# Kernel tuning notes

Hardware: AMD Instinct MI355X
Metric: run time of the kernel (lower is better)

The kernel has to match this reference:

```python
import jax, jax.numpy as jnp
import numpy as np

B, T, C = 4, 2048, 1024
N_HEAD = 16
HEAD_DIM = C // N_HEAD
SCALE = 1.0 / np.sqrt(HEAD_DIM).astype(np.float32)


def setup_inputs() -> dict:
    key = jax.random.key(0)
    ks = jax.random.split(key, 5)
    std = 1.0 / np.sqrt(C).astype(np.float32)
    return {
        "x": jax.random.normal(ks[0], (B, T, C), dtype=jnp.float32),
        "Wq": jax.random.normal(ks[1], (C, C), dtype=jnp.float32) * std,
        "Wk": jax.random.normal(ks[2], (C, C), dtype=jnp.float32) * std,
        "Wv": jax.random.normal(ks[3], (C, C), dtype=jnp.float32) * std,
        "Wo": jax.random.normal(ks[4], (C, C), dtype=jnp.float32) * std,
    }


def reference(x, Wq, Wk, Wv, Wo):
    # nn.Linear(x) == x @ W.T; projections then split heads: (B, H, T, D)
    def split_heads(t):
        return t.reshape(B, T, N_HEAD, HEAD_DIM).transpose(0, 2, 1, 3)

    q = split_heads(x @ Wq.T)
    k = split_heads(x @ Wk.T)
    v = split_heads(x @ Wv.T)

    att = jnp.einsum("bhqd,bhkd->bhqk", q, k) * SCALE  # (B, H, T, T)
    causal = jnp.tril(jnp.ones((T, T), dtype=bool))
    att = jnp.where(causal[None, None], att, -jnp.inf)
    att = jax.nn.softmax(att, axis=-1)
    # dropout = 0.0 (eval): identity
    y = jnp.einsum("bhqk,bhkd->bhqd", att, v)  # (B, H, T, D)
    y = y.transpose(0, 2, 1, 3).reshape(B, T, C)
    return y @ Wo.T
```

## Files before the change

kernel.cpp:

```cpp
#include <hip/hip_runtime.h>
#include <stdint.h>

#define B_SZ   4
#define T_SEQ  2048
#define C_DIM  1024
#define N_HEAD 16
#define HEAD_D 64
#define QSCALE 0.18033688011112042f
#define M_FIX  12.0f

typedef unsigned short u16;
typedef unsigned int   u32;
typedef __bf16  bfv8  __attribute__((ext_vector_type(8)));
typedef float   f32x4 __attribute__((ext_vector_type(4)));

__device__ __forceinline__ u16 f2bf_hu(float f) {
  union { float f; u32 i; } u; u.f = f;
  return (u16)((u.i + 0x8000u) >> 16);
}
__device__ __forceinline__ u32 pkbf16(float a, float b) {
  union { float f; u32 i; } ua, ub; ua.f = a; ub.f = b;
  return ((ua.i + 0x8000u) >> 16) | ((ub.i + 0x8000u) & 0xFFFF0000u);
}
__device__ __forceinline__ float fexp2(float x) {
#if __has_builtin(__builtin_amdgcn_exp2f)
  return __builtin_amdgcn_exp2f(x);
#else
  return __expf(x * 0.69314718f);
#endif
}

__device__ __forceinline__ void async_cp16(const u16* __restrict__ g, u16* l) {
  __builtin_amdgcn_global_load_lds(
      (const __attribute__((address_space(1))) void*)g,
      (__attribute__((address_space(3))) void*)l, 16, 0, 0);
}

__global__ __launch_bounds__(256) void cvt_kernel(const float* __restrict__ src,
                                                  u16* __restrict__ dst, int n4) {
  int i = blockIdx.x * 256 + threadIdx.x;
  if (i < n4) {
    float4 v = ((const float4*)src)[i];
    int2 o; o.x = (int)pkbf16(v.x, v.y); o.y = (int)pkbf16(v.z, v.w);
    ((int2*)dst)[i] = o;
  }
}
__global__ __launch_bounds__(256) void cvt_w_kernel(
    const float* __restrict__ W0, const float* __restrict__ W1,
    const float* __restrict__ W2, const float* __restrict__ W3,
    u16* __restrict__ dst) {
  const float* s = (blockIdx.y == 0) ? W0 : (blockIdx.y == 1) ? W1
                 : (blockIdx.y == 2) ? W2 : W3;
  u16* d = dst + (size_t)blockIdx.y * (C_DIM * C_DIM);
  int i = blockIdx.x * 256 + threadIdx.x;
  float4 v = ((const float4*)s)[i];
  int2 o; o.x = (int)pkbf16(v.x, v.y); o.y = (int)pkbf16(v.z, v.w);
  ((int2*)d)[i] = o;
}

__device__ __forceinline__ void mfma_step(const u16* Sbuf, int wm, int wn,
                                          int frow, int fk, f32x4 acc[4][4]) {
  const u16* As = Sbuf;
  const u16* Bs = Sbuf + 4096;
  bfv8 af[4], bfr[4];
#pragma unroll
  for (int mt = 0; mt < 4; mt++)
    af[mt] = *(const bfv8*)(As + (wm * 64 + mt * 16 + frow) * 32 + fk);
#pragma unroll
  for (int nt = 0; nt < 4; nt++)
    bfr[nt] = *(const bfv8*)(Bs + (wn * 64 + nt * 16 + frow) * 32 + fk);
#pragma unroll
  for (int mt = 0; mt < 4; mt++)
#pragma unroll
    for (int nt = 0; nt < 4; nt++)
      acc[mt][nt] = __builtin_amdgcn_mfma_f32_16x16x32_bf16(
          af[mt], bfr[nt], acc[mt][nt], 0, 0, 0);
}

__device__ __forceinline__ void gemm_core(const u16* __restrict__ A,
                                          const u16* __restrict__ Bw,
                                          int m0, int n0,
                                          f32x4 acc[4][4],
                                          u16* smem) {
  const int tid  = threadIdx.x;
  const int wave = tid >> 6;
  const int lane = tid & 63;
  const int frow = lane & 15;
  const int fk   = (lane >> 4) * 8;
  const int wm   = wave >> 1, wn = wave & 1;

  const int lrow = tid >> 2;
  const int lcol = (tid & 3) * 8;
  const u16* ga0 = A  + (size_t)(m0 + lrow)      * C_DIM + lcol;
  const u16* ga1 = A  + (size_t)(m0 + 64 + lrow) * C_DIM + lcol;
  const u16* gb0 = Bw + (size_t)(n0 + lrow)      * C_DIM + lcol;
  const u16* gb1 = Bw + (size_t)(n0 + 64 + lrow) * C_DIM + lcol;
  u16* b0 = smem;
  u16* b1 = smem + 8192;
  const int so = tid * 8;

#define STAGE_TO(dst) do {                        \
    async_cp16(ga0, (dst) + so);                  \
    async_cp16(ga1, (dst) + 2048 + so);           \
    async_cp16(gb0, (dst) + 4096 + so);           \
    async_cp16(gb1, (dst) + 6144 + so);           \
    ga0 += 32; ga1 += 32; gb0 += 32; gb1 += 32;   \
  } while (0)

  STAGE_TO(b0);
  __syncthreads();

  for (int it = 0; it < 32; it += 2) {
    STAGE_TO(b1);
    mfma_step(b0, wm, wn, frow, fk, acc);
    __syncthreads();
    if (it < 30) STAGE_TO(b0);
    mfma_step(b1, wm, wn, frow, fk, acc);
    __syncthreads();
  }
#undef STAGE_TO
}

__global__ __launch_bounds__(256) void gemm_qkv_kernel(
    const u16* __restrict__ X, const u16* __restrict__ Wq,
    const u16* __restrict__ Wk, const u16* __restrict__ Wv,
    u16* __restrict__ Qo, u16* __restrict__ Ko, u16* __restrict__ Vo) {
  __shared__ __align__(16) u16 smem[16384];
  const u16* W = (blockIdx.z == 0) ? Wq : (blockIdx.z == 1) ? Wk : Wv;
  u16* dst     = (blockIdx.z == 0) ? Qo : (blockIdx.z == 1) ? Ko : Vo;
  const int m0 = blockIdx.x * 128, n0 = blockIdx.y * 128;

  f32x4 acc[4][4];
#pragma unroll
  for (int i = 0; i < 4; i++)
#pragma unroll
    for (int j = 0; j < 4; j++) acc[i][j] = {0.f, 0.f, 0.f, 0.f};

  gemm_core(X, W, m0, n0, acc, smem);
  __syncthreads();

  const int lane = threadIdx.x & 63, wave = threadIdx.x >> 6;
  const int wm = wave >> 1, wn = wave & 1;
  const int quad = lane >> 4, col = lane & 15;
  u16* buf = smem + wave * 4096;
  const int bb = (m0 + wm * 64) >> 11;
  const int t0 = (m0 + wm * 64) & (T_SEQ - 1);
  const int h  = (n0 >> 6) + wn;

  if (blockIdx.z == 2) {
#pragma unroll
    for (int mt = 0; mt < 4; mt++)
#pragma unroll
      for (int nt = 0; nt < 4; nt++) {
        int d_l = nt * 16 + col;
        int g   = mt * 4 + quad;
        int gp  = g ^ (d_l & 15);
        int2 o;
        o.x = (int)pkbf16(acc[mt][nt][0], acc[mt][nt][1]);
        o.y = (int)pkbf16(acc[mt][nt][2], acc[mt][nt][3]);
        *(int2*)(buf + d_l * 64 + gp * 4) = o;
      }
#pragma unroll
    for (int tt = 0; tt < 8; tt++) {
      int d_l = tt * 8 + (lane >> 3);
      int seg = lane & 7;
      int g0 = (2 * seg) ^ (d_l & 15), g1 = (2 * seg + 1) ^ (d_l & 15);
      int2 a  = *(const int2*)(buf + d_l * 64 + g0 * 4);
      int2 bv = *(const int2*)(buf + d_l * 64 + g1 * 4);
      int4 o; o.x = a.x; o.y = a.y; o.z = bv.x; o.w = bv.y;
      *(int4*)(Vo + (((size_t)(bb * N_HEAD + h) * HEAD_D + d_l) * T_SEQ
                     + t0 + seg * 8)) = o;
    }
  } else {
    const float sc = (blockIdx.z == 0) ? QSCALE : 1.0f;
#pragma unroll
    for (int mt = 0; mt < 4; mt++)
#pragma unroll
      for (int nt = 0; nt < 4; nt++)
#pragma unroll
        for (int r = 0; r < 4; r++) {
          int m_l = mt * 16 + quad * 4 + r;
          int n_l = nt * 16 + col;
          int gp = (n_l >> 3) ^ (m_l & 7);
          buf[m_l * 64 + gp * 8 + (n_l & 7)] = f2bf_hu(acc[mt][nt][r] * sc);
        }
#pragma unroll
    for (int tt = 0; tt < 8; tt++) {
      int m_l = tt * 8 + (lane >> 3);
      int seg = lane & 7;
      int gp = seg ^ (m_l & 7);
      int4 o = *(const int4*)(buf + m_l * 64 + gp * 8);
      *(int4*)(dst + (((size_t)(bb * N_HEAD + h) * T_SEQ + t0 + m_l) * HEAD_D
                      + seg * 8)) = o;
    }
  }
}

__global__ __launch_bounds__(256) void gemm_out_kernel(
    const u16* __restrict__ Y, const u16* __restrict__ Wo,
    float* __restrict__ Out) {
  __shared__ __align__(16) u16 smem[16384];
  const int m0 = blockIdx.x * 128, n0 = blockIdx.y * 128;

  f32x4 acc[4][4];
#pragma unroll
  for (int i = 0; i < 4; i++)
#pragma unroll
    for (int j = 0; j < 4; j++) acc[i][j] = {0.f, 0.f, 0.f, 0.f};

  gemm_core(Y, Wo, m0, n0, acc, smem);
  __syncthreads();

  const int lane = threadIdx.x & 63, wave = threadIdx.x >> 6;
  const int wm = wave >> 1, wn = wave & 1;
  const int quad = lane >> 4, col = lane & 15;
  float* bufF = (float*)(smem + wave * 4096);

#pragma unroll
  for (int c = 0; c < 2; c++) {
#pragma unroll
    for (int mt = 0; mt < 4; mt++)
#pragma unroll
      for (int nn = 0; nn < 2; nn++)
#pragma unroll
        for (int r = 0; r < 4; r++) {
          int nt = 2 * c + nn;
          int m_l = mt * 16 + quad * 4 + r;
          int n_l = nn * 16 + col;
          int gp = (n_l >> 2) ^ (m_l & 7);
          bufF[m_l * 32 + gp * 4 + (n_l & 3)] = acc[mt][nt][r];
        }
#pragma unroll
    for (int tt = 0; tt < 8; tt++) {
      int m_l = tt * 8 + (lane >> 3);
      int seg = lane & 7;
      int gp = seg ^ (m_l & 7);
      float4 o = *(const float4*)(bufF + m_l * 32 + gp * 4);
      *(float4*)(Out + (size_t)(m0 + wm * 64 + m_l) * C_DIM
                 + n0 + wn * 64 + c * 32 + seg * 4) = o;
    }
  }
}

#define ATT_Q 128

__global__ __launch_bounds__(256, 4) void attn_kernel(
    const u16* __restrict__ Qg, const u16* __restrict__ Kg,
    const u16* __restrict__ Vtg, u16* __restrict__ Yg) {
  __shared__ __align__(16) u16 QPs[128 * 64];
  __shared__ __align__(16) u16 Ks[64 * 64];
  __shared__ __align__(16) u16 Vt[64 * 64];

  const int tid = threadIdx.x;
  const int wave = tid >> 6, lane = tid & 63;
  const int quad = lane >> 4, l15 = lane & 15;
  const int bh = blockIdx.x;
  const int b = bh >> 4, h = bh & 15;
  const int yy = blockIdx.y, gq = yy >> 2, rq = yy & 3;
  const int qt = (gq == 0) ? 15 - rq : (gq == 1) ? rq
               : (gq == 2) ? 11 - rq : 4 + rq;
  const int q0 = qt * ATT_Q;

  {
    const int row = tid >> 1;
    const int c0 = (tid & 1) * 32;
    const u16* gp = Qg + ((size_t)bh * T_SEQ + q0 + row) * HEAD_D + c0;
#pragma unroll
    for (int g = 0; g < 4; g++) {
      int4 v = *(const int4*)(gp + g * 8);
      int pg = ((c0 >> 3) + g) ^ (row & 7);
      *(int4*)(QPs + row * 64 + pg * 8) = v;
    }
  }
  __syncthreads();

  bfv8 qb[2][2];
#pragma unroll
  for (int nt = 0; nt < 2; nt++)
#pragma unroll
    for (int ks = 0; ks < 2; ks++) {
      int q = wave * 32 + nt * 16 + l15;
      int pg = (ks * 4 + quad) ^ (q & 7);
      qb[nt][ks] = *(const bfv8*)(QPs + q * 64 + pg * 8);
    }

  float l_i[2] = {0.f, 0.f};
  f32x4 ao[4][2];
#pragma unroll
  for (int mt = 0; mt < 4; mt++)
#pragma unroll
    for (int nt = 0; nt < 2; nt++) ao[mt][nt] = {0.f, 0.f, 0.f, 0.f};

  const int srow = tid >> 2;
  const int sc0 = (tid & 3) * 16;
  const u16* gkb = Kg  + (size_t)bh * T_SEQ * HEAD_D + (size_t)srow * HEAD_D + sc0;
  const u16* gvb = Vtg + (size_t)bh * HEAD_D * T_SEQ + (size_t)srow * T_SEQ + sc0;
  const int pg0 = (sc0 >> 3) ^ (srow & 7), pg1 = ((sc0 >> 3) + 1) ^ (srow & 7);

  int4 kr0, kr1, vr0, vr1;
  kr0 = *(const int4*)(gkb);      kr1 = *(const int4*)(gkb + 8);
  vr0 = *(const int4*)(gvb);      vr1 = *(const int4*)(gvb + 8);

  const int ktmax = 2 * qt + 1;
  for (int kt = 0; kt <= ktmax; kt++) {
    __syncthreads();
    *(int4*)(Ks + srow * 64 + pg0 * 8) = kr0;
    *(int4*)(Ks + srow * 64 + pg1 * 8) = kr1;
    *(int4*)(Vt + srow * 64 + pg0 * 8) = vr0;
    *(int4*)(Vt + srow * 64 + pg1 * 8) = vr1;
    __syncthreads();
    if (kt < ktmax) {
      const u16* gk = gkb + (size_t)(kt + 1) * 64 * HEAD_D;
      const u16* gv = gvb + (kt + 1) * 64;
      kr0 = *(const int4*)(gk);  kr1 = *(const int4*)(gk + 8);
      vr0 = *(const int4*)(gv);  vr1 = *(const int4*)(gv + 8);
    }

    f32x4 as[4][2];
#pragma unroll
    for (int mt = 0; mt < 4; mt++)
#pragma unroll
      for (int nt = 0; nt < 2; nt++) as[mt][nt] = {0.f, 0.f, 0.f, 0.f};
#pragma unroll
    for (int mt = 0; mt < 4; mt++) {
      bfv8 ka[2];
#pragma unroll
      for (int ks = 0; ks < 2; ks++) {
        int key = mt * 16 + l15;
        int pg = (ks * 4 + quad) ^ (key & 7);
        ka[ks] = *(const bfv8*)(Ks + key * 64 + pg * 8);
      }
#pragma unroll
      for (int nt = 0; nt < 2; nt++)
#pragma unroll
        for (int ks = 0; ks < 2; ks++)
          as[mt][nt] = __builtin_amdgcn_mfma_f32_16x16x32_bf16(
              ka[ks], qb[nt][ks], as[mt][nt], 0, 0, 0);
    }

    const bool diag = (kt >= 2 * qt);
#pragma unroll
    for (int nt = 0; nt < 2; nt++) {
      const int q_l = wave * 32 + nt * 16 + l15;
      const int q_g = q0 + q_l;
      float lacc = 0.f;
#pragma unroll
      for (int mt = 0; mt < 4; mt++) {
        float p[4];
#pragma unroll
        for (int r = 0; r < 4; r++) {
          float s = as[mt][nt][r];
          if (diag) {
            int key_g = kt * 64 + mt * 16 + quad * 4 + r;
            if (key_g > q_g) s = -1e30f;
          }
          p[r] = fexp2(s - M_FIX);
        }
        lacc += (p[0] + p[1]) + (p[2] + p[3]);
        int pg = (2 * mt + (quad >> 1)) ^ (q_l & 7);
        int2 o;
        o.x = (int)pkbf16(p[0], p[1]);
        o.y = (int)pkbf16(p[2], p[3]);
        *(int2*)(QPs + q_l * 64 + pg * 8 + (quad & 1) * 4) = o;
      }
      l_i[nt] += lacc;
    }

    bfv8 pf[2][2];
#pragma unroll
    for (int nt = 0; nt < 2; nt++)
#pragma unroll
      for (int ks = 0; ks < 2; ks++) {
        int q_l = wave * 32 + nt * 16 + l15;
        int pg = (ks * 4 + quad) ^ (q_l & 7);
        pf[nt][ks] = *(const bfv8*)(QPs + q_l * 64 + pg * 8);
      }
#pragma unroll
    for (int mt = 0; mt < 4; mt++) {
      bfv8 va[2];
#pragma unroll
      for (int ks = 0; ks < 2; ks++) {
        int d = mt * 16 + l15;
        int pg = (ks * 4 + quad) ^ (d & 7);
        va[ks] = *(const bfv8*)(Vt + d * 64 + pg * 8);
      }
#pragma unroll
      for (int nt = 0; nt < 2; nt++)
#pragma unroll
        for (int ks = 0; ks < 2; ks++)
          ao[mt][nt] = __builtin_amdgcn_mfma_f32_16x16x32_bf16(
              va[ks], pf[nt][ks], ao[mt][nt], 0, 0, 0);
    }
  }

#pragma unroll
  for (int nt = 0; nt < 2; nt++) {
    l_i[nt] += __shfl_xor(l_i[nt], 16);
    l_i[nt] += __shfl_xor(l_i[nt], 32);
  }

  __syncthreads();
#pragma unroll
  for (int nt = 0; nt < 2; nt++) {
    float inv = 1.0f / l_i[nt];
    int q_l = wave * 32 + nt * 16 + l15;
#pragma unroll
    for (int mt = 0; mt < 4; mt++) {
      int g = mt * 4 + quad;
      int gp = g ^ (q_l & 15);
      int2 o;
      o.x = (int)pkbf16(ao[mt][nt][0] * inv, ao[mt][nt][1] * inv);
      o.y = (int)pkbf16(ao[mt][nt][2] * inv, ao[mt][nt][3] * inv);
      *(int2*)(QPs + q_l * 64 + gp * 4) = o;
    }
  }
  __syncthreads();
#pragma unroll
  for (int rr = 0; rr < 4; rr++) {
    int q   = rr * 32 + (tid >> 3);
    int seg = tid & 7;
    int g0 = (2 * seg) ^ (q & 15), g1 = (2 * seg + 1) ^ (q & 15);
    int2 a  = *(const int2*)(QPs + q * 64 + g0 * 4);
    int2 bv = *(const int2*)(QPs + q * 64 + g1 * 4);
    int4 o; o.x = a.x; o.y = a.y; o.z = bv.x; o.w = bv.y;
    *(int4*)(Yg + ((size_t)b * T_SEQ + q0 + q) * C_DIM + h * HEAD_D + seg * 8) = o;
  }
}

extern "C" void kernel_launch(void* const* d_in, const int* in_sizes, int n_in,
                              void* d_out, int out_size, void* d_ws, size_t ws_size,
                              hipStream_t stream) {
  const float* x  = (const float*)d_in[0];
  const float* Wq = (const float*)d_in[1];
  const float* Wk = (const float*)d_in[2];
  const float* Wv = (const float*)d_in[3];
  const float* Wo = (const float*)d_in[4];
  float* out = (float*)d_out;

  const size_t NE = (size_t)B_SZ * T_SEQ * C_DIM;
  const size_t NW = (size_t)C_DIM * C_DIM;
  u16* xbf = (u16*)d_ws;
  u16* wqb = xbf + NE;
  u16* wkb = wqb + NW;
  u16* wvb = wkb + NW;
  u16* wob = wvb + NW;
  u16* qws = wob + NW;
  u16* kws = qws + NE;
  u16* vws = kws + NE;
  u16* yws = vws + NE;

  cvt_kernel<<<(int)(NE / 4 / 256), 256, 0, stream>>>(x, xbf, (int)(NE / 4));
  cvt_w_kernel<<<dim3((int)(NW / 4 / 256), 4), 256, 0, stream>>>(Wq, Wk, Wv, Wo, wqb);

  dim3 g1(T_SEQ * B_SZ / 128, C_DIM / 128, 3);
  gemm_qkv_kernel<<<g1, 256, 0, stream>>>(xbf, wqb, wkb, wvb, qws, kws, vws);

  dim3 g2(B_SZ * N_HEAD, T_SEQ / ATT_Q);
  attn_kernel<<<g2, 256, 0, stream>>>(qws, kws, vws, yws);

  dim3 g3(T_SEQ * B_SZ / 128, C_DIM / 128);
  gemm_out_kernel<<<g3, 256, 0, stream>>>(yws, wob, out);
}
```

Baseline: 246.6 us.

## Deepen GEMM async-copy pipeline from double to quad buffering

Turns the shared GEMM core's two-buffer staging into a four-buffer ring. Two k-stages are prefetched ahead, and a partial vmcnt wait allows one stage's global loads to stay in flight across each barrier. This is meant to hide global-to-LDS latency better in both the QKV and output projection GEMMs. In exchange the LDS footprint doubles to 64KB per block, which may cut occupancy, and the hand-written waitcnt counts must match the number of outstanding copies.

```diff
diff --git a/kernel.cpp b/kernel.cpp
--- a/kernel.cpp
+++ b/kernel.cpp
@@ -97,6 +97,8 @@
   const u16* gb1 = Bw + (size_t)(n0 + 64 + lrow) * C_DIM + lcol;
   u16* b0 = smem;
   u16* b1 = smem + 8192;
+  u16* b2 = smem + 16384;
+  u16* b3 = smem + 24576;
   const int so = tid * 8;
 
 #define STAGE_TO(dst) do {                        \
@@ -106,26 +108,49 @@
     async_cp16(gb1, (dst) + 6144 + so);           \
     ga0 += 32; ga1 += 32; gb0 += 32; gb1 += 32;   \
   } while (0)
+#define WAIT4_BAR do {                                      \
+    asm volatile("s_waitcnt vmcnt(4)" ::: "memory");        \
+    __builtin_amdgcn_s_barrier();                           \
+  } while (0)
 
   STAGE_TO(b0);
-  __syncthreads();
-
-  for (int it = 0; it < 32; it += 2) {
-    STAGE_TO(b1);
+  STAGE_TO(b1);
+  WAIT4_BAR;
+
+#pragma unroll 1
+  for (int ii = 0; ii < 32; ii += 4) {
+    const bool more = (ii < 28);
+
+    STAGE_TO(b2);
     mfma_step(b0, wm, wn, frow, fk, acc);
-    __syncthreads();
-    if (it < 30) STAGE_TO(b0);
+    WAIT4_BAR;
+
+    STAGE_TO(b3);
     mfma_step(b1, wm, wn, frow, fk, acc);
-    __syncthreads();
+    WAIT4_BAR;
+
+    if (more) STAGE_TO(b0);
+    mfma_step(b2, wm, wn, frow, fk, acc);
+    if (more) {
+      asm volatile("s_waitcnt vmcnt(4)" ::: "memory");
+    } else {
+      asm volatile("s_waitcnt vmcnt(0)" ::: "memory");
+    }
+    __builtin_amdgcn_s_barrier();
+
+    if (more) STAGE_TO(b1);
+    mfma_step(b3, wm, wn, frow, fk, acc);
+    if (more) WAIT4_BAR;
   }
 #undef STAGE_TO
+#undef WAIT4_BAR
 }
 
 __global__ __launch_bounds__(256) void gemm_qkv_kernel(
     const u16* __restrict__ X, const u16* __restrict__ Wq,
     const u16* __restrict__ Wk, const u16* __restrict__ Wv,
     u16* __restrict__ Qo, u16* __restrict__ Ko, u16* __restrict__ Vo) {
-  __shared__ __align__(16) u16 smem[16384];
+  __shared__ __align__(16) u16 smem[32768];
   const u16* W = (blockIdx.z == 0) ? Wq : (blockIdx.z == 1) ? Wk : Wv;
   u16* dst     = (blockIdx.z == 0) ? Qo : (blockIdx.z == 1) ? Ko : Vo;
   const int m0 = blockIdx.x * 128, n0 = blockIdx.y * 128;
@@ -199,7 +224,7 @@
 __global__ __launch_bounds__(256) void gemm_out_kernel(
     const u16* __restrict__ Y, const u16* __restrict__ Wo,
     float* __restrict__ Out) {
-  __shared__ __align__(16) u16 smem[16384];
+  __shared__ __align__(16) u16 smem[32768];
   const int m0 = blockIdx.x * 128, n0 = blockIdx.y * 128;
 
   f32x4 acc[4][4];
```

New measurement: 239.1 us. -3.0%, faster.
